# Kernel optimization log

Hardware: AMD Instinct MI355X
Metric: run time of the kernel (lower is better)

## Reference

```python
import jax, jax.numpy as jnp
import numpy as np

D_MODEL = 1024
N_HEADS = 16
HEAD_DIM = D_MODEL // N_HEADS
THETA = 10000.0
B, S = 4, 2048


def setup_inputs() -> dict:
    key = jax.random.key(0)
    ks = jax.random.split(key, 5)
    scale = 1.0 / np.sqrt(D_MODEL)
    x = jax.random.normal(ks[0], (B, S, D_MODEL), dtype=jnp.float32)
    token_positions = jnp.broadcast_to(jnp.arange(S, dtype=jnp.int32)[None, :], (B, S))
    WQ = jax.random.normal(ks[1], (D_MODEL, D_MODEL), dtype=jnp.float32) * scale
    WK = jax.random.normal(ks[2], (D_MODEL, D_MODEL), dtype=jnp.float32) * scale
    WV = jax.random.normal(ks[3], (D_MODEL, D_MODEL), dtype=jnp.float32) * scale
    WO = jax.random.normal(ks[4], (D_MODEL, D_MODEL), dtype=jnp.float32) * scale
    return {"x": x, "token_positions": token_positions, "WQ": WQ, "WK": WK, "WV": WV, "WO": WO}


def _apply_rope(t, token_positions):
    # t: [b, h, s, d]; token_positions: [b, s]
    d = t.shape[-1]
    inv_freq = THETA ** (-jnp.arange(0, d, 2, dtype=jnp.float32) / d)  # [d/2]
    ang = token_positions.astype(jnp.float32)[:, None, :, None] * inv_freq  # [b,1,s,d/2]
    cos, sin = jnp.cos(ang), jnp.sin(ang)
    t_even, t_odd = t[..., 0::2], t[..., 1::2]
    r_even = t_even * cos - t_odd * sin
    r_odd = t_even * sin + t_odd * cos
    out = jnp.stack([r_even, r_odd], axis=-1)  # interleave pairs back
    return out.reshape(t.shape)


def reference(x, token_positions, WQ, WK, WV, WO):
    b, s, _ = x.shape
    def proj(W):
        y = jnp.einsum('bsd,ed->bse', x, W)  # Linear: x @ W^T, W is [out,in]
        return y.reshape(b, s, N_HEADS, HEAD_DIM).transpose(0, 2, 1, 3)  # [b,h,s,d]
    Q = _apply_rope(proj(WQ), token_positions)
    K = _apply_rope(proj(WK), token_positions)
    V = proj(WV)
    scores = jnp.einsum('bhqd,bhkd->bhqk', Q, K) / jnp.sqrt(jnp.float32(HEAD_DIM))
    causal = jnp.tril(jnp.ones((s, s), dtype=bool))
    scores = jnp.where(causal, scores, -jnp.inf)
    attn = jax.nn.softmax(scores, axis=-1)
    out = jnp.einsum('bhqk,bhkd->bhqd', attn, V)
    out = out.transpose(0, 2, 1, 3).reshape(b, s, D_MODEL)
    return jnp.einsum('bse,oe->bso', out, WO)
```

## Files before the change

kernel.cpp:

```cpp
#include <hip/hip_runtime.h>

typedef __bf16 bf16x8 __attribute__((ext_vector_type(8)));
typedef __bf16 bf16x2 __attribute__((ext_vector_type(2)));
typedef float f32x4 __attribute__((ext_vector_type(4)));
typedef float f32x2 __attribute__((ext_vector_type(2)));
typedef unsigned short u16;
typedef unsigned int u32;

#define MFMA16(a, b, c) __builtin_amdgcn_mfma_f32_16x16x32_bf16((a), (b), (c), 0, 0, 0)

__device__ __forceinline__ u16 f2b(float f) {
  u32 u = __float_as_uint(f);
  u += 0x7FFFu + ((u >> 16) & 1u);
  return (u16)(u >> 16);
}
__device__ __forceinline__ float b2f(u16 h) { return __uint_as_float(((u32)h) << 16); }

__device__ __forceinline__ u32 pkbf(float a, float b) {
  bf16x2 h = {(__bf16)a, (__bf16)b};
  return __builtin_bit_cast(u32, h);
}

__device__ __forceinline__ float max3f(float a, float b, float c) {
  float d;
  asm("v_max3_f32 %0, %1, %2, %3" : "=v"(d) : "v"(a), "v"(b), "v"(c));
  return d;
}

__device__ __forceinline__ float exp2_(float x) {
#if __has_builtin(__builtin_amdgcn_exp2f)
  return __builtin_amdgcn_exp2f(x);
#else
  return exp2f(x);
#endif
}

__device__ __forceinline__ void glds16(const void* g, void* l) {
  __builtin_amdgcn_global_load_lds((const __attribute__((address_space(1))) void*)g,
                                   (__attribute__((address_space(3))) void*)l, 16, 0, 0);
}

__global__ __launch_bounds__(256) void cvt_k(const float* __restrict__ x,
                                             const float* __restrict__ wq,
                                             const float* __restrict__ wk,
                                             const float* __restrict__ wv,
                                             const float* __restrict__ wo,
                                             u16* __restrict__ dst) {
  size_t e = ((size_t)blockIdx.x * 256 + threadIdx.x) * 4;
  const float* src;
  size_t off;
  if (e < 8388608ull) {
    src = x; off = e;
  } else {
    size_t r = e - 8388608ull;
    u32 wi = (u32)(r >> 20);
    off = r & 1048575ull;
    src = (wi == 0) ? wq : (wi == 1) ? wk : (wi == 2) ? wv : wo;
  }
  float4 v = *(const float4*)(src + off);
  ushort4 o = make_ushort4(f2b(v.x), f2b(v.y), f2b(v.z), f2b(v.w));
  *(ushort4*)(dst + e) = o;
}

__global__ __launch_bounds__(256) void rope_tab_k(const int* __restrict__ pos,
                                                  float2* __restrict__ tab) {
  int i = blockIdx.x * 256 + threadIdx.x;
  int row = i >> 5, j = i & 31;
  float p = (float)pos[row];
  float inv = exp2f((float)j * -0.41524101186092029f);
  float s, c;
  sincosf(p * inv, &s, &c);
  tab[i] = make_float2(c, s);
}

__global__ __launch_bounds__(512, 2) void gemm_qkv_k(const u16* __restrict__ Xb,
                                                     const u16* __restrict__ Wq,
                                                     const u16* __restrict__ Wk,
                                                     const u16* __restrict__ Wv,
                                                     const float2* __restrict__ tab,
                                                     u16* __restrict__ Qp,
                                                     u16* __restrict__ Kp,
                                                     u16* __restrict__ Vt) {
  __shared__ u16 As[3][16384];
  __shared__ u16 Bs[3][8192];
  const int wgid = blockIdx.x;
  const int xcd = wgid & 7;
  const int idx = wgid >> 3;
  const int P = xcd * 12 + (idx >> 3);
  const int nt = idx & 7;
  const int z = P >> 5;
  const int mt = P & 31;
  const u16* W = (z == 0) ? Wq : (z == 1) ? Wk : Wv;
  const int t = threadIdx.x;
  const int wave = t >> 6, lane = t & 63;
  const int lr = lane & 15, lg = lane >> 4;
  const int wr = wave >> 1, wc = wave & 1;

  const int srow = t >> 3;
  const int scc = t & 7;
  const int ssw = scc ^ (srow & 7);
  const u16* aA = Xb + (size_t)(mt * 256 + srow) * 1024 + ssw * 8;
  const u16* bB = W + (size_t)(nt * 128 + srow) * 1024 + ssw * 8;

  f32x4 acc[4][4];
#pragma unroll
  for (int i = 0; i < 4; ++i)
#pragma unroll
    for (int j = 0; j < 4; ++j) acc[i][j] = (f32x4){0.f, 0.f, 0.f, 0.f};

#pragma unroll
  for (int tt = 0; tt < 2; ++tt) {
    const int kt = tt * 64;
    glds16(aA + kt, &As[tt][t * 8]);
    glds16(aA + 64 * 1024 + kt, &As[tt][4096 + t * 8]);
    glds16(bB + kt, &Bs[tt][t * 8]);
    glds16(aA + 128 * 1024 + kt, &As[tt][8192 + t * 8]);
    glds16(aA + 192 * 1024 + kt, &As[tt][12288 + t * 8]);
    glds16(bB + 64 * 1024 + kt, &Bs[tt][4096 + t * 8]);
  }
  asm volatile("s_waitcnt vmcnt(6)" ::: "memory");
  __builtin_amdgcn_s_barrier();

  const int arow = (wr * 64 + lr) * 64;
  const int brow = (wc * 64 + lr) * 64;
  const int sw = lr & 7;

  int sl = 0;
  for (int tau = 0; tau < 16; ++tau) {
    const int sp2 = (sl + 2 >= 3) ? sl - 1 : sl + 2;
    const u16* Asl = &As[sl][0];
    const u16* Bsl = &Bs[sl][0];
    u16* Ad = &As[sp2][0];
    u16* Bd = &Bs[sp2][0];
    const int kt2 = (tau + 2) * 64;
    bf16x8 af[4], bf[4];

    {
      const int koff = (lg ^ sw) * 8;
#pragma unroll
      for (int mi = 0; mi < 4; ++mi)
        af[mi] = *(const bf16x8*)&Asl[arow + mi * 1024 + koff];
#pragma unroll
      for (int nj = 0; nj < 4; ++nj)
        bf[nj] = *(const bf16x8*)&Bsl[brow + nj * 1024 + koff];
    }
    if (tau < 14) {
      glds16(aA + kt2, &Ad[t * 8]);
      glds16(aA + 64 * 1024 + kt2, &Ad[4096 + t * 8]);
      glds16(bB + kt2, &Bd[t * 8]);
    }
    __builtin_amdgcn_s_barrier();
    asm volatile("s_waitcnt lgkmcnt(0)" ::: "memory");
    __builtin_amdgcn_sched_barrier(0);
    __builtin_amdgcn_s_setprio(1);
#pragma unroll
    for (int mi = 0; mi < 4; ++mi)
#pragma unroll
      for (int nj = 0; nj < 4; ++nj)
        acc[mi][nj] = MFMA16(af[mi], bf[nj], acc[mi][nj]);
    __builtin_amdgcn_s_setprio(0);
    __builtin_amdgcn_sched_barrier(0);
    __builtin_amdgcn_s_barrier();

    {
      const int koff = ((4 + lg) ^ sw) * 8;
#pragma unroll
      for (int mi = 0; mi < 4; ++mi)
        af[mi] = *(const bf16x8*)&Asl[arow + mi * 1024 + koff];
#pragma unroll
      for (int nj = 0; nj < 4; ++nj)
        bf[nj] = *(const bf16x8*)&Bsl[brow + nj * 1024 + koff];
    }
    if (tau < 14) {
      glds16(aA + 128 * 1024 + kt2, &Ad[8192 + t * 8]);
      glds16(aA + 192 * 1024 + kt2, &Ad[12288 + t * 8]);
      glds16(bB + 64 * 1024 + kt2, &Bd[4096 + t * 8]);
    }
    __builtin_amdgcn_s_barrier();
    asm volatile("s_waitcnt lgkmcnt(0)" ::: "memory");
    __builtin_amdgcn_sched_barrier(0);
    __builtin_amdgcn_s_setprio(1);
#pragma unroll
    for (int mi = 0; mi < 4; ++mi)
#pragma unroll
      for (int nj = 0; nj < 4; ++nj)
        acc[mi][nj] = MFMA16(af[mi], bf[nj], acc[mi][nj]);
    __builtin_amdgcn_s_setprio(0);
    __builtin_amdgcn_sched_barrier(0);
    if (tau < 14) asm volatile("s_waitcnt vmcnt(6)" ::: "memory");
    else asm volatile("s_waitcnt vmcnt(0)" ::: "memory");
    __builtin_amdgcn_s_barrier();
    sl = (sl == 2) ? 0 : sl + 1;
  }

  const int rbase = mt * 256 + wr * 64 + lg * 4;
  const int cbase = nt * 128 + wc * 64 + lr;
  if (z < 2) {
    u16* out = (z == 0) ? Qp : Kp;
    const float scl = (z == 0) ? 0.18033688011112043f : 1.0f;
#pragma unroll
    for (int mi = 0; mi < 4; ++mi)
#pragma unroll
      for (int nj = 0; nj < 4; ++nj) {
        int row0 = rbase + mi * 16;
        int col = cbase + nj * 16;
        int j = (col >> 1) & 31;
        float sgn = (col & 1) ? 1.f : -1.f;
#pragma unroll
        for (int r = 0; r < 4; ++r) {
          float self = acc[mi][nj][r];
          float partner = __shfl_xor(self, 1);
          float2 cs = tab[(size_t)(row0 + r) * 32 + j];
          float o = (self * cs.x + partner * cs.y * sgn) * scl;
          out[(size_t)(row0 + r) * 1024 + col] = f2b(o);
        }
      }
  } else {
#pragma unroll
    for (int mi = 0; mi < 4; ++mi)
#pragma unroll
      for (int nj = 0; nj < 4; ++nj) {
        int row0 = rbase + mi * 16;
        int e = cbase + nj * 16;
        int b = row0 >> 11, s = row0 & 2047;
        ushort4 pk = make_ushort4(f2b(acc[mi][nj][0]), f2b(acc[mi][nj][1]),
                                  f2b(acc[mi][nj][2]), f2b(acc[mi][nj][3]));
        *(ushort4*)&Vt[((size_t)(b * 1024 + e)) * 2048 + s] = pk;
      }
  }
}

__global__ __launch_bounds__(512, 4) void fattn_k(const u16* __restrict__ Qp,
                                                  const u16* __restrict__ Kp,
                                                  const u16* __restrict__ Vt,
                                                  u16* __restrict__ Ao) {
  __shared__ u16 Ks[2][64 * 64];
  __shared__ u16 Vs[2][64 * 64];
  __shared__ u16 Ps[8][16 * 64];
  const int blk = blockIdx.x;
  const int g = blk & 7, jj = blk >> 3;
  const int bh = g * 8 + (jj & 7);
  const int J = jj >> 3;
  const int qt = (J < 4) ? (7 - J) : (J - 4);
  const int b = bh >> 4, h = bh & 15;
  const int tid = threadIdx.x, wave = tid >> 6, lane = tid & 63;
  const int lr = lane & 15, lg = lane >> 4;
  const int q0w = qt * 256 + wave * 32;

  bf16x8 qf[2][2];
#pragma unroll
  for (int qh = 0; qh < 2; ++qh) {
    const u16* qb = Qp + ((size_t)(b * 2048 + q0w + qh * 16 + lr)) * 1024 + h * 64 + lg * 8;
    qf[qh][0] = *(const bf16x8*)qb;
    qf[qh][1] = *(const bf16x8*)(qb + 32);
  }

  float m[2], l[2];
  f32x4 oacc[2][4];
#pragma unroll
  for (int qh = 0; qh < 2; ++qh) {
    m[qh] = -1e30f; l[qh] = 0.f;
#pragma unroll
    for (int d4 = 0; d4 < 4; ++d4) oacc[qh][d4] = (f32x4){0.f, 0.f, 0.f, 0.f};
  }
  const f32x4 fz = {0.f, 0.f, 0.f, 0.f};

  const int srow = lane >> 3;
  const int schunk = (lane & 7) ^ srow;
  const u16* kbase = Kp + ((size_t)(b * 2048 + 8 * wave + srow)) * 1024 + h * 64 + schunk * 8;
  const u16* vbase = Vt + ((size_t)(b * 1024 + h * 64 + 8 * wave + srow)) * 2048 + schunk * 8;
  char* psbase = (char*)&Ps[wave][0];

  const int ktmax = 4 * qt + 3;
  const int ktneed = 4 * qt + (wave >> 1);

  glds16(kbase, &Ks[0][(8 * wave) * 64]);
  glds16(vbase, &Vs[0][(8 * wave) * 64]);

  int cur = 0;
  for (int kt = 0; kt <= ktmax; ++kt, cur ^= 1) {
    __syncthreads();
    if (kt < ktmax) {
      const int nx = cur ^ 1, k1 = kt + 1;
      glds16(kbase + (size_t)k1 * 65536, &Ks[nx][(8 * wave) * 64]);
      glds16(vbase + k1 * 64, &Vs[nx][(8 * wave) * 64]);
    }
    if (kt > ktneed) continue;
    const u16* KB = &Ks[cur][0];
    const u16* VB = &Vs[cur][0];

    f32x4 sc[2][4];
#pragma unroll
    for (int ks = 0; ks < 4; ++ks) {
      const int krow = ks * 16 + lr;
      const int swk = lr & 7;
      bf16x8 kf0 = *(const bf16x8*)&KB[krow * 64 + ((lg ^ swk) * 8)];
      bf16x8 kf1 = *(const bf16x8*)&KB[krow * 64 + (((lg + 4) ^ swk) * 8)];
#pragma unroll
      for (int qh = 0; qh < 2; ++qh) {
        f32x4 s = MFMA16(kf0, qf[qh][0], fz);
        s = MFMA16(kf1, qf[qh][1], s);
        sc[qh][ks] = s;
      }
    }
    if (kt == ktneed) {
#pragma unroll
      for (int qh = 0; qh < 2; ++qh) {
        int q = q0w + qh * 16 + lr;
#pragma unroll
        for (int ks = 0; ks < 4; ++ks)
#pragma unroll
          for (int r = 0; r < 4; ++r) {
            int kv = kt * 64 + ks * 16 + lg * 4 + r;
            if (kv > q) sc[qh][ks][r] = -__builtin_inff();
          }
      }
    }

#pragma unroll
    for (int qh = 0; qh < 2; ++qh) {
      float t0 = max3f(sc[qh][0][0], sc[qh][0][1], sc[qh][0][2]);
      float t1 = max3f(sc[qh][0][3], sc[qh][1][0], sc[qh][1][1]);
      float t2 = max3f(sc[qh][1][2], sc[qh][1][3], sc[qh][2][0]);
      float t3 = max3f(sc[qh][2][1], sc[qh][2][2], sc[qh][2][3]);
      float t4 = max3f(sc[qh][3][0], sc[qh][3][1], sc[qh][3][2]);
      float pm = max3f(max3f(t0, t1, t2), max3f(t3, t4, sc[qh][3][3]),
                       -1e30f);
      pm = fmaxf(pm, __shfl_xor(pm, 16));
      pm = fmaxf(pm, __shfl_xor(pm, 32));
      if (__any(pm > m[qh] + 8.f)) {
        float mn = fmaxf(m[qh], pm);
        float corr = exp2_(m[qh] - mn);
        m[qh] = mn;
        l[qh] *= corr;
        float cb[4];
#pragma unroll
        for (int r = 0; r < 4; ++r) cb[r] = __shfl(corr, (lane & 48) | (lg * 4 + r));
#pragma unroll
        for (int d4 = 0; d4 < 4; ++d4)
#pragma unroll
          for (int r = 0; r < 4; ++r) oacc[qh][d4][r] *= cb[r];
      }
      const f32x2 ms = {m[qh], m[qh]};
      f32x2 rs2 = {0.f, 0.f};
#pragma unroll
      for (int ks = 0; ks < 4; ++ks) {
        f32x2 lo = {sc[qh][ks][0], sc[qh][ks][1]};
        f32x2 hi = {sc[qh][ks][2], sc[qh][ks][3]};
        lo = lo - ms;
        hi = hi - ms;
        lo[0] = exp2_(lo[0]); lo[1] = exp2_(lo[1]);
        hi[0] = exp2_(hi[0]); hi[1] = exp2_(hi[1]);
        rs2 += lo;
        rs2 += hi;
        sc[qh][ks][0] = lo[0]; sc[qh][ks][1] = lo[1];
        sc[qh][ks][2] = hi[0]; sc[qh][ks][3] = hi[1];
      }
      float rs = rs2[0] + rs2[1];
      rs += __shfl_xor(rs, 16);
      rs += __shfl_xor(rs, 32);
      l[qh] += rs;
    }

    bf16x8 pa[2][2];
#pragma unroll
    for (int qh = 0; qh < 2; ++qh) {
      const int swp = lr & 7;
#pragma unroll
      for (int ks = 0; ks < 4; ++ks) {
        const int chunk = (2 * ks + (lg >> 1)) ^ swp;
        char* p = psbase + lr * 128 + chunk * 16 + (lg & 1) * 8;
        *(uint2*)p = make_uint2(pkbf(sc[qh][ks][0], sc[qh][ks][1]),
                                pkbf(sc[qh][ks][2], sc[qh][ks][3]));
      }
      pa[qh][0] = *(const bf16x8*)(psbase + lr * 128 + ((lg ^ swp) * 16));
      pa[qh][1] = *(const bf16x8*)(psbase + lr * 128 + (((lg + 4) ^ swp) * 16));
    }
#pragma unroll
    for (int d4 = 0; d4 < 4; ++d4) {
      const int vrow = d4 * 16 + lr;
      const int swv = lr & 7;
      bf16x8 vf0 = *(const bf16x8*)&VB[vrow * 64 + ((lg ^ swv) * 8)];
      bf16x8 vf1 = *(const bf16x8*)&VB[vrow * 64 + (((lg + 4) ^ swv) * 8)];
      oacc[0][d4] = MFMA16(pa[0][0], vf0, oacc[0][d4]);
      oacc[0][d4] = MFMA16(pa[0][1], vf1, oacc[0][d4]);
      oacc[1][d4] = MFMA16(pa[1][0], vf0, oacc[1][d4]);
      oacc[1][d4] = MFMA16(pa[1][1], vf1, oacc[1][d4]);
    }
  }

#pragma unroll
  for (int qh = 0; qh < 2; ++qh) {
    float lb[4];
#pragma unroll
    for (int r = 0; r < 4; ++r) lb[r] = __shfl(l[qh], (lane & 48) | (lg * 4 + r));
#pragma unroll
    for (int r = 0; r < 4; ++r) {
      float inv = 1.f / lb[r];
      int q = q0w + qh * 16 + lg * 4 + r;
      u16* orow = Ao + ((size_t)(b * 2048 + q)) * 1024 + h * 64 + lr;
#pragma unroll
      for (int d4 = 0; d4 < 4; ++d4) orow[d4 * 16] = f2b(oacc[qh][d4][r] * inv);
    }
  }
}

__global__ __launch_bounds__(512, 2) void gemm_wo_k(const u16* __restrict__ Ab,
                                                    const u16* __restrict__ Wo,
                                                    float* __restrict__ Out) {
  __shared__ u16 As[3][16384];
  __shared__ u16 Bs[3][8192];
  const int wgid = blockIdx.x;
  const int xcd = wgid & 7;
  const int idx = wgid >> 3;
  const int mt = xcd * 4 + (idx >> 3);
  const int nt = idx & 7;
  const int t = threadIdx.x;
  const int wave = t >> 6, lane = t & 63;
  const int lr = lane & 15, lg = lane >> 4;
  const int wr = wave >> 1, wc = wave & 1;

  const int srow = t >> 3;
  const int scc = t & 7;
  const int ssw = scc ^ (srow & 7);
  const u16* aA = Ab + (size_t)(mt * 256 + srow) * 1024 + ssw * 8;
  const u16* bB = Wo + (size_t)(nt * 128 + srow) * 1024 + ssw * 8;

  f32x4 acc[4][4];
#pragma unroll
  for (int i = 0; i < 4; ++i)
#pragma unroll
    for (int j = 0; j < 4; ++j) acc[i][j] = (f32x4){0.f, 0.f, 0.f, 0.f};

#pragma unroll
  for (int tt = 0; tt < 2; ++tt) {
    const int kt = tt * 64;
    glds16(aA + kt, &As[tt][t * 8]);
    glds16(aA + 64 * 1024 + kt, &As[tt][4096 + t * 8]);
    glds16(bB + kt, &Bs[tt][t * 8]);
    glds16(aA + 128 * 1024 + kt, &As[tt][8192 + t * 8]);
    glds16(aA + 192 * 1024 + kt, &As[tt][12288 + t * 8]);
    glds16(bB + 64 * 1024 + kt, &Bs[tt][4096 + t * 8]);
  }
  asm volatile("s_waitcnt vmcnt(6)" ::: "memory");
  __builtin_amdgcn_s_barrier();

  const int arow = (wr * 64 + lr) * 64;
  const int brow = (wc * 64 + lr) * 64;
  const int sw = lr & 7;

  int sl = 0;
  for (int tau = 0; tau < 16; ++tau) {
    const int sp2 = (sl + 2 >= 3) ? sl - 1 : sl + 2;
    const u16* Asl = &As[sl][0];
    const u16* Bsl = &Bs[sl][0];
    u16* Ad = &As[sp2][0];
    u16* Bd = &Bs[sp2][0];
    const int kt2 = (tau + 2) * 64;
    bf16x8 af[4], bf[4];

    {
      const int koff = (lg ^ sw) * 8;
#pragma unroll
      for (int mi = 0; mi < 4; ++mi)
        af[mi] = *(const bf16x8*)&Asl[arow + mi * 1024 + koff];
#pragma unroll
      for (int nj = 0; nj < 4; ++nj)
        bf[nj] = *(const bf16x8*)&Bsl[brow + nj * 1024 + koff];
    }
    if (tau < 14) {
      glds16(aA + kt2, &Ad[t * 8]);
      glds16(aA + 64 * 1024 + kt2, &Ad[4096 + t * 8]);
      glds16(bB + kt2, &Bd[t * 8]);
    }
    __builtin_amdgcn_s_barrier();
    asm volatile("s_waitcnt lgkmcnt(0)" ::: "memory");
    __builtin_amdgcn_sched_barrier(0);
    __builtin_amdgcn_s_setprio(1);
#pragma unroll
    for (int mi = 0; mi < 4; ++mi)
#pragma unroll
      for (int nj = 0; nj < 4; ++nj)
        acc[mi][nj] = MFMA16(af[mi], bf[nj], acc[mi][nj]);
    __builtin_amdgcn_s_setprio(0);
    __builtin_amdgcn_sched_barrier(0);
    __builtin_amdgcn_s_barrier();

    {
      const int koff = ((4 + lg) ^ sw) * 8;
#pragma unroll
      for (int mi = 0; mi < 4; ++mi)
        af[mi] = *(const bf16x8*)&Asl[arow + mi * 1024 + koff];
#pragma unroll
      for (int nj = 0; nj < 4; ++nj)
        bf[nj] = *(const bf16x8*)&Bsl[brow + nj * 1024 + koff];
    }
    if (tau < 14) {
      glds16(aA + 128 * 1024 + kt2, &Ad[8192 + t * 8]);
      glds16(aA + 192 * 1024 + kt2, &Ad[12288 + t * 8]);
      glds16(bB + 64 * 1024 + kt2, &Bd[4096 + t * 8]);
    }
    __builtin_amdgcn_s_barrier();
    asm volatile("s_waitcnt lgkmcnt(0)" ::: "memory");
    __builtin_amdgcn_sched_barrier(0);
    __builtin_amdgcn_s_setprio(1);
#pragma unroll
    for (int mi = 0; mi < 4; ++mi)
#pragma unroll
      for (int nj = 0; nj < 4; ++nj)
        acc[mi][nj] = MFMA16(af[mi], bf[nj], acc[mi][nj]);
    __builtin_amdgcn_s_setprio(0);
    __builtin_amdgcn_sched_barrier(0);
    if (tau < 14) asm volatile("s_waitcnt vmcnt(6)" ::: "memory");
    else asm volatile("s_waitcnt vmcnt(0)" ::: "memory");
    __builtin_amdgcn_s_barrier();
    sl = (sl == 2) ? 0 : sl + 1;
  }

  const int rbase = mt * 256 + wr * 64 + lg * 4;
  const int cbase = nt * 128 + wc * 64 + lr;
#pragma unroll
  for (int mi = 0; mi < 4; ++mi)
#pragma unroll
    for (int nj = 0; nj < 4; ++nj) {
      int row0 = rbase + mi * 16;
      int col = cbase + nj * 16;
#pragma unroll
      for (int r = 0; r < 4; ++r)
        Out[(size_t)(row0 + r) * 1024 + col] = acc[mi][nj][r];
    }
}

extern "C" void kernel_launch(void* const* d_in, const int* in_sizes, int n_in,
                              void* d_out, int out_size, void* d_ws, size_t ws_size,
                              hipStream_t stream) {
  const float* x = (const float*)d_in[0];
  const int* pos = (const int*)d_in[1];
  const float* wq = (const float*)d_in[2];
  const float* wk = (const float*)d_in[3];
  const float* wv = (const float*)d_in[4];
  const float* wo = (const float*)d_in[5];

  char* ws = (char*)d_ws;
  u16* xb = (u16*)ws;
  u16* wqb = xb + 8388608;
  u16* wkb = wqb + 1048576;
  u16* wvb = wkb + 1048576;
  u16* wob = wvb + 1048576;
  float2* tab = (float2*)(ws + 25165824);
  u16* Qp = (u16*)(ws + 27262976);
  u16* Kp = (u16*)(ws + 27262976 + 16777216);
  u16* Vt = (u16*)(ws + 27262976 + 2 * 16777216);
  u16* Ao = (u16*)(ws + 27262976 + 3 * 16777216);

  hipLaunchKernelGGL(cvt_k, dim3(12288), dim3(256), 0, stream, x, wq, wk, wv, wo, xb);
  hipLaunchKernelGGL(rope_tab_k, dim3(1024), dim3(256), 0, stream, pos, tab);
  hipLaunchKernelGGL(gemm_qkv_k, dim3(768), dim3(512), 0, stream, xb, wqb, wkb, wvb,
                     tab, Qp, Kp, Vt);
  hipLaunchKernelGGL(fattn_k, dim3(512), dim3(512), 0, stream, Qp, Kp, Vt, Ao);
  hipLaunchKernelGGL(gemm_wo_k, dim3(256), dim3(512), 0, stream, Ao, wob, (float*)d_out);
}
```

Before: 174.7 us.

## Shrink QKV GEMM tile to 128x128 with 256 threads and K-step 32

The QKV projection GEMM drops from 256x128 tiles with 8 waves to 128x128 tiles with 4 waves. The K step per stage shrinks from 64 to 32, giving 32 iterations with a single MFMA phase and one barrier each. The shared-memory swizzle and load mapping are reworked to match, and the grid doubles to 1536 blocks so each CU can hold three workgroups. The aim is better occupancy and fewer barriers per MFMA, at the cost of less operand reuse per tile and more global traffic for the X and weight loads.

```diff
diff --git a/kernel.cpp b/kernel.cpp
--- a/kernel.cpp
+++ b/kernel.cpp
@@ -73,7 +73,7 @@
   tab[i] = make_float2(c, s);
 }
 
-__global__ __launch_bounds__(512, 2) void gemm_qkv_k(const u16* __restrict__ Xb,
+__global__ __launch_bounds__(256, 3) void gemm_qkv_k(const u16* __restrict__ Xb,
                                                      const u16* __restrict__ Wq,
                                                      const u16* __restrict__ Wk,
                                                      const u16* __restrict__ Wv,
@@ -81,26 +81,28 @@
                                                      u16* __restrict__ Qp,
                                                      u16* __restrict__ Kp,
                                                      u16* __restrict__ Vt) {
-  __shared__ u16 As[3][16384];
-  __shared__ u16 Bs[3][8192];
+  __shared__ u16 As[3][4096];
+  __shared__ u16 Bs[3][4096];
   const int wgid = blockIdx.x;
   const int xcd = wgid & 7;
   const int idx = wgid >> 3;
-  const int P = xcd * 12 + (idx >> 3);
+  const int P = xcd * 24 + (idx >> 3);
   const int nt = idx & 7;
-  const int z = P >> 5;
-  const int mt = P & 31;
+  const int z = P >> 6;
+  const int mt = P & 63;
   const u16* W = (z == 0) ? Wq : (z == 1) ? Wk : Wv;
   const int t = threadIdx.x;
   const int wave = t >> 6, lane = t & 63;
   const int lr = lane & 15, lg = lane >> 4;
   const int wr = wave >> 1, wc = wave & 1;
 
-  const int srow = t >> 3;
-  const int scc = t & 7;
-  const int ssw = scc ^ (srow & 7);
-  const u16* aA = Xb + (size_t)(mt * 256 + srow) * 1024 + ssw * 8;
-  const u16* bB = W + (size_t)(nt * 128 + srow) * 1024 + ssw * 8;
+  const int rr0 = t >> 3;
+  const int s8 = t & 7;
+  const int sl8 = s8 ^ (rr0 & 7);
+  const int js = sl8 >> 2;
+  const int kcs = sl8 & 3;
+  const u16* aS = Xb + (size_t)(mt * 128 + rr0 + 64 * js) * 1024 + kcs * 8;
+  const u16* bS = W + (size_t)(nt * 128 + rr0 + 64 * js) * 1024 + kcs * 8;
 
   f32x4 acc[4][4];
 #pragma unroll
@@ -110,46 +112,36 @@
 
 #pragma unroll
   for (int tt = 0; tt < 2; ++tt) {
-    const int kt = tt * 64;
-    glds16(aA + kt, &As[tt][t * 8]);
-    glds16(aA + 64 * 1024 + kt, &As[tt][4096 + t * 8]);
-    glds16(bB + kt, &Bs[tt][t * 8]);
-    glds16(aA + 128 * 1024 + kt, &As[tt][8192 + t * 8]);
-    glds16(aA + 192 * 1024 + kt, &As[tt][12288 + t * 8]);
-    glds16(bB + 64 * 1024 + kt, &Bs[tt][4096 + t * 8]);
-  }
-  asm volatile("s_waitcnt vmcnt(6)" ::: "memory");
+    const int kcol = tt * 32;
+    glds16(aS + kcol, &As[tt][t * 8]);
+    glds16(aS + 32 * 1024 + kcol, &As[tt][2048 + t * 8]);
+    glds16(bS + kcol, &Bs[tt][t * 8]);
+    glds16(bS + 32 * 1024 + kcol, &Bs[tt][2048 + t * 8]);
+  }
+  asm volatile("s_waitcnt vmcnt(4)" ::: "memory");
   __builtin_amdgcn_s_barrier();
 
-  const int arow = (wr * 64 + lr) * 64;
-  const int brow = (wc * 64 + lr) * 64;
-  const int sw = lr & 7;
-
-  int sl = 0;
-  for (int tau = 0; tau < 16; ++tau) {
-    const int sp2 = (sl + 2 >= 3) ? sl - 1 : sl + 2;
+  const int arb = lr * 64 + (((wr << 2) + lg) ^ (lr & 7)) * 8;
+  const int brb = lr * 64 + (((wc << 2) + lg) ^ (lr & 7)) * 8;
+
+  int sl = 0, sp2 = 2;
+  for (int tau = 0; tau < 32; ++tau) {
     const u16* Asl = &As[sl][0];
     const u16* Bsl = &Bs[sl][0];
-    u16* Ad = &As[sp2][0];
-    u16* Bd = &Bs[sp2][0];
-    const int kt2 = (tau + 2) * 64;
     bf16x8 af[4], bf[4];
-
-    {
-      const int koff = (lg ^ sw) * 8;
-#pragma unroll
-      for (int mi = 0; mi < 4; ++mi)
-        af[mi] = *(const bf16x8*)&Asl[arow + mi * 1024 + koff];
-#pragma unroll
-      for (int nj = 0; nj < 4; ++nj)
-        bf[nj] = *(const bf16x8*)&Bsl[brow + nj * 1024 + koff];
-    }
-    if (tau < 14) {
-      glds16(aA + kt2, &Ad[t * 8]);
-      glds16(aA + 64 * 1024 + kt2, &Ad[4096 + t * 8]);
-      glds16(bB + kt2, &Bd[t * 8]);
-    }
-    __builtin_amdgcn_s_barrier();
+#pragma unroll
+    for (int mi = 0; mi < 4; ++mi) af[mi] = *(const bf16x8*)&Asl[arb + mi * 1024];
+#pragma unroll
+    for (int nj = 0; nj < 4; ++nj) bf[nj] = *(const bf16x8*)&Bsl[brb + nj * 1024];
+    if (tau < 30) {
+      u16* Ad = &As[sp2][0];
+      u16* Bd = &Bs[sp2][0];
+      const int kcol = (tau + 2) * 32;
+      glds16(aS + kcol, &Ad[t * 8]);
+      glds16(aS + 32 * 1024 + kcol, &Ad[2048 + t * 8]);
+      glds16(bS + kcol, &Bd[t * 8]);
+      glds16(bS + 32 * 1024 + kcol, &Bd[2048 + t * 8]);
+    }
     asm volatile("s_waitcnt lgkmcnt(0)" ::: "memory");
     __builtin_amdgcn_sched_barrier(0);
     __builtin_amdgcn_s_setprio(1);
@@ -160,40 +152,14 @@
         acc[mi][nj] = MFMA16(af[mi], bf[nj], acc[mi][nj]);
     __builtin_amdgcn_s_setprio(0);
     __builtin_amdgcn_sched_barrier(0);
-    __builtin_amdgcn_s_barrier();
-
-    {
-      const int koff = ((4 + lg) ^ sw) * 8;
-#pragma unroll
-      for (int mi = 0; mi < 4; ++mi)
-        af[mi] = *(const bf16x8*)&Asl[arow + mi * 1024 + koff];
-#pragma unroll
-      for (int nj = 0; nj < 4; ++nj)
-        bf[nj] = *(const bf16x8*)&Bsl[brow + nj * 1024 + koff];
-    }
-    if (tau < 14) {
-      glds16(aA + 128 * 1024 + kt2, &Ad[8192 + t * 8]);
-      glds16(aA + 192 * 1024 + kt2, &Ad[12288 + t * 8]);
-      glds16(bB + 64 * 1024 + kt2, &Bd[4096 + t * 8]);
-    }
-    __builtin_amdgcn_s_barrier();
-    asm volatile("s_waitcnt lgkmcnt(0)" ::: "memory");
-    __builtin_amdgcn_sched_barrier(0);
-    __builtin_amdgcn_s_setprio(1);
-#pragma unroll
-    for (int mi = 0; mi < 4; ++mi)
-#pragma unroll
-      for (int nj = 0; nj < 4; ++nj)
-        acc[mi][nj] = MFMA16(af[mi], bf[nj], acc[mi][nj]);
-    __builtin_amdgcn_s_setprio(0);
-    __builtin_amdgcn_sched_barrier(0);
-    if (tau < 14) asm volatile("s_waitcnt vmcnt(6)" ::: "memory");
+    if (tau < 30) asm volatile("s_waitcnt vmcnt(4)" ::: "memory");
     else asm volatile("s_waitcnt vmcnt(0)" ::: "memory");
     __builtin_amdgcn_s_barrier();
     sl = (sl == 2) ? 0 : sl + 1;
-  }
-
-  const int rbase = mt * 256 + wr * 64 + lg * 4;
+    sp2 = (sp2 == 2) ? 0 : sp2 + 1;
+  }
+
+  const int rbase = mt * 128 + wr * 64 + lg * 4;
   const int cbase = nt * 128 + wc * 64 + lr;
   if (z < 2) {
     u16* out = (z == 0) ? Qp : Kp;
@@ -555,7 +521,7 @@
 
   hipLaunchKernelGGL(cvt_k, dim3(12288), dim3(256), 0, stream, x, wq, wk, wv, wo, xb);
   hipLaunchKernelGGL(rope_tab_k, dim3(1024), dim3(256), 0, stream, pos, tab);
-  hipLaunchKernelGGL(gemm_qkv_k, dim3(768), dim3(512), 0, stream, xb, wqb, wkb, wvb,
+  hipLaunchKernelGGL(gemm_qkv_k, dim3(1536), dim3(256), 0, stream, xb, wqb, wkb, wvb,
                      tab, Qp, Kp, Vt);
   hipLaunchKernelGGL(fattn_k, dim3(512), dim3(512), 0, stream, Qp, Kp, Vt, Ao);
   hipLaunchKernelGGL(gemm_wo_k, dim3(256), dim3(512), 0, stream, Ao, wob, (float*)d_out);
```

Result: no change. 172.9 us (-1.0%).
